# Performance work log

Measured on AMD Instinct MI355X. Metric: run time of the kernel, lower is better.

The kernel has to match this reference:

```python
import jax, jax.numpy as jnp
import numpy as np

N_NODES = 100000
N_EDGES = 1000000
D_IN, H1, H2, D_OUT = 64, 64, 32, 16


def gcn_conv(x, W, b, src, dst, n):
    # PyG GCNConv: add self-loops, symmetric normalization deg^-1/2 A deg^-1/2, then linear.
    h = x @ W  # [N, out]
    ones = jnp.ones(src.shape[0], dtype=x.dtype)
    deg = jax.ops.segment_sum(ones, dst, num_segments=n) + 1.0  # +1 for self-loop
    dinv = jnp.where(deg > 0, jax.lax.rsqrt(deg), 0.0)
    coef = dinv[src] * dinv[dst]  # [E]
    msg = h[src] * coef[:, None]  # [E, out]
    agg = jax.ops.segment_sum(msg, dst, num_segments=n)
    agg = agg + h * (dinv * dinv)[:, None]  # self-loop contribution
    return agg + b


def setup_inputs() -> dict:
    key = jax.random.key(0)
    ks = jax.random.split(key, 16)
    s = 0.1
    inp = {
        "x": jax.random.normal(ks[0], (N_NODES, D_IN), jnp.float32),
        "edge_index": jax.random.randint(ks[1], (2, N_EDGES), 0, N_NODES, jnp.int64),
        # SELayer params
        "U_w": jax.random.normal(ks[2], (D_IN, D_IN), jnp.float32) * s,
        "U_b": jnp.zeros((D_IN,), jnp.float32),
        "fc1_w": jax.random.normal(ks[3], (D_IN, D_IN // 4), jnp.float32) * s,
        "fc1_b": jnp.zeros((D_IN // 4,), jnp.float32),
        "fc2_w": jax.random.normal(ks[4], (D_IN // 4, D_IN), jnp.float32) * s,
        "fc2_b": jnp.zeros((D_IN,), jnp.float32),
        # GCN layers
        "W1": jax.random.normal(ks[5], (D_IN, H1), jnp.float32) * s,
        "b1": jnp.zeros((H1,), jnp.float32),
        "W2": jax.random.normal(ks[6], (H1, H2), jnp.float32) * s,
        "b2": jnp.zeros((H2,), jnp.float32),
        # classifier
        "fc_w": jax.random.normal(ks[7], (H2, D_OUT), jnp.float32) * s,
        "fc_b": jnp.zeros((D_OUT,), jnp.float32),
    }
    return inp


def reference(x, edge_index, U_w, U_b, fc1_w, fc1_b, fc2_w, fc2_b, W1, b1, W2, b2, fc_w, fc_b):
    n = x.shape[0]
    src, dst = edge_index[0], edge_index[1]
    # SE layer
    xu = x @ U_w + U_b
    w = jax.nn.sigmoid(jax.nn.relu(xu @ fc1_w + fc1_b) @ fc2_w + fc2_b)
    h = xu * w
    # GCN stack (dropout is identity in eval mode)
    h = jax.nn.relu(gcn_conv(h, W1, b1, src, dst, n))
    h = jax.nn.relu(gcn_conv(h, W2, b2, src, dst, n))
    logits = h @ fc_w + fc_b
    return jax.nn.log_softmax(logits, axis=1), w
```

## Files before the change

kernel.cpp:

```cpp
#include <hip/hip_runtime.h>
#include <hip/hip_bf16.h>

#define NN 100000
#define NE 1000000
#define CAP 64

#define NPER 196
#define GRID_FAT (NPER * 13)

__device__ __forceinline__ float f4c(const float4& v, int i) {
    switch (i) { case 0: return v.x; case 1: return v.y; case 2: return v.z; default: return v.w; }
}
__device__ __forceinline__ unsigned short f2bf(float f) {
    unsigned u = __float_as_uint(f);
    return (unsigned short)((u + 0x7FFFu + ((u >> 16) & 1u)) >> 16);
}
__device__ __forceinline__ float bf2f(unsigned short s) {
    return __uint_as_float(((unsigned)s) << 16);
}

__global__ __launch_bounds__(256) void zero_k(int* __restrict__ bucket)
{
    long i = (long)blockIdx.x * 256 + threadIdx.x;
    if (i < NN) bucket[i * CAP] = 0;
}

__global__ __launch_bounds__(256) void fat_kernel(
    const float* __restrict__ x, const void* __restrict__ eidx,
    const float* __restrict__ U_w, const float* __restrict__ U_b,
    const float* __restrict__ f1w, const float* __restrict__ f1b,
    const float* __restrict__ f2w, const float* __restrict__ f2b,
    const float* __restrict__ W1,
    int* __restrict__ bucket,
    unsigned short* __restrict__ hW1b, float* __restrict__ w_out)
{
    const int b = blockIdx.x;
    const int r13 = b % 13;
    const int tid = threadIdx.x;

    if (r13 < 5) {
        const int sidx = (b / 13) * 5 + r13;
        long e0 = ((long)sidx * 256 + tid) * 4;
        if (e0 >= NE) return;

        const unsigned* pp = (const unsigned*)eidx;
        bool is64 = true;
#pragma unroll
        for (int k = 0; k < 8; ++k)
            if (pp[2 * k + 1] != 0u) is64 = false;

        int srcs[4], dsts[4];
        if (is64) {
            const long long* p = (const long long*)eidx;
#pragma unroll
            for (int i = 0; i < 4; ++i) {
                srcs[i] = (int)p[e0 + i];
                dsts[i] = (int)p[NE + e0 + i];
            }
        } else {
            const int* p = (const int*)eidx;
            int4 s4 = *(const int4*)&p[e0];
            int4 d4 = *(const int4*)&p[NE + e0];
            srcs[0] = s4.x; srcs[1] = s4.y; srcs[2] = s4.z; srcs[3] = s4.w;
            dsts[0] = d4.x; dsts[1] = d4.y; dsts[2] = d4.z; dsts[3] = d4.w;
        }

        int pos[4];
#pragma unroll
        for (int i = 0; i < 4; ++i) pos[i] = atomicAdd(&bucket[dsts[i] * CAP], 1);
#pragma unroll
        for (int i = 0; i < 4; ++i)
            if (pos[i] < CAP - 1) bucket[dsts[i] * CAP + 1 + pos[i]] = srcs[i];
        return;
    }

    const int seidx = (b / 13) * 8 + (r13 - 5);
    const long base = (long)seidx * 64;
    if (base >= NN) return;

    __shared__ float sU[64][68];
    __shared__ float sx[64][68];
    __shared__ float st1[64][20];
    __shared__ float sUb[64], sb1[16], sb2[64];

    for (int i = tid; i < 1024; i += 256) {
        int r = i >> 4, q = i & 15;
        *(float4*)&sU[r][q * 4] = *(const float4*)&U_w[r * 64 + q * 4];
    }
    for (int i = tid; i < 1024; i += 256) {
        int r = i >> 4, q = i & 15;
        long row = base + r;
        float4 v = make_float4(0.f, 0.f, 0.f, 0.f);
        if (row < NN) v = *(const float4*)&x[row * 64 + q * 4];
        *(float4*)&sx[r][q * 4] = v;
    }
    if (tid < 64) sUb[tid] = U_b[tid];
    if (tid < 16) sb1[tid] = f1b[tid];
    if (tid < 64) sb2[tid] = f2b[tid];
    __syncthreads();

    const int cg = tid & 15, rg = tid >> 4;
    const int r0 = rg * 4, c0 = cg * 4;

    float acc[4][4];
#pragma unroll
    for (int ri = 0; ri < 4; ++ri)
#pragma unroll
        for (int ci = 0; ci < 4; ++ci) acc[ri][ci] = 0.f;

#pragma unroll 4
    for (int kk = 0; kk < 64; kk += 4) {
        float4 xa[4];
#pragma unroll
        for (int ri = 0; ri < 4; ++ri) xa[ri] = *(float4*)&sx[r0 + ri][kk];
#pragma unroll
        for (int kq = 0; kq < 4; ++kq) {
            float4 ub = *(float4*)&sU[kk + kq][c0];
#pragma unroll
            for (int ri = 0; ri < 4; ++ri) {
                float xv = f4c(xa[ri], kq);
                acc[ri][0] = fmaf(xv, ub.x, acc[ri][0]);
                acc[ri][1] = fmaf(xv, ub.y, acc[ri][1]);
                acc[ri][2] = fmaf(xv, ub.z, acc[ri][2]);
                acc[ri][3] = fmaf(xv, ub.w, acc[ri][3]);
            }
        }
    }
    __syncthreads();

#pragma unroll
    for (int ri = 0; ri < 4; ++ri) {
        acc[ri][0] += sUb[c0 + 0];
        acc[ri][1] += sUb[c0 + 1];
        acc[ri][2] += sUb[c0 + 2];
        acc[ri][3] += sUb[c0 + 3];
        float4 o = make_float4(acc[ri][0], acc[ri][1], acc[ri][2], acc[ri][3]);
        *(float4*)&sx[r0 + ri][c0] = o;
    }
    __syncthreads();

    float a1[4] = {sb1[cg], sb1[cg], sb1[cg], sb1[cg]};
#pragma unroll 4
    for (int kk = 0; kk < 64; kk += 4) {
        float4 xa[4];
#pragma unroll
        for (int ri = 0; ri < 4; ++ri) xa[ri] = *(float4*)&sx[r0 + ri][kk];
#pragma unroll
        for (int kq = 0; kq < 4; ++kq) {
            float wv = f1w[(kk + kq) * 16 + cg];
#pragma unroll
            for (int ri = 0; ri < 4; ++ri) a1[ri] = fmaf(f4c(xa[ri], kq), wv, a1[ri]);
        }
    }
#pragma unroll
    for (int ri = 0; ri < 4; ++ri) st1[r0 + ri][cg] = fmaxf(a1[ri], 0.f);
    __syncthreads();

    float a2[4][4];
#pragma unroll
    for (int ri = 0; ri < 4; ++ri)
#pragma unroll
        for (int ci = 0; ci < 4; ++ci) a2[ri][ci] = sb2[c0 + ci];

#pragma unroll
    for (int kk = 0; kk < 16; kk += 4) {
        float4 ta[4];
#pragma unroll
        for (int ri = 0; ri < 4; ++ri) ta[ri] = *(float4*)&st1[r0 + ri][kk];
#pragma unroll
        for (int kq = 0; kq < 4; ++kq) {
            float4 fb = *(const float4*)&f2w[(kk + kq) * 64 + c0];
#pragma unroll
            for (int ri = 0; ri < 4; ++ri) {
                float xv = f4c(ta[ri], kq);
                a2[ri][0] = fmaf(xv, fb.x, a2[ri][0]);
                a2[ri][1] = fmaf(xv, fb.y, a2[ri][1]);
                a2[ri][2] = fmaf(xv, fb.z, a2[ri][2]);
                a2[ri][3] = fmaf(xv, fb.w, a2[ri][3]);
            }
        }
    }
#pragma unroll
    for (int ri = 0; ri < 4; ++ri) {
        long row = base + r0 + ri;
        float4 wv;
        wv.x = 1.f / (1.f + expf(-a2[ri][0]));
        wv.y = 1.f / (1.f + expf(-a2[ri][1]));
        wv.z = 1.f / (1.f + expf(-a2[ri][2]));
        wv.w = 1.f / (1.f + expf(-a2[ri][3]));
        float4 h4;
        h4.x = acc[ri][0] * wv.x; h4.y = acc[ri][1] * wv.y;
        h4.z = acc[ri][2] * wv.z; h4.w = acc[ri][3] * wv.w;
        *(float4*)&sx[r0 + ri][c0] = h4;
        if (row < NN) *(float4*)&w_out[row * 64 + c0] = wv;
    }
    for (int i = tid; i < 1024; i += 256) {
        int r = i >> 4, q = i & 15;
        *(float4*)&sU[r][q * 4] = *(const float4*)&W1[r * 64 + q * 4];
    }
    __syncthreads();

#pragma unroll
    for (int ri = 0; ri < 4; ++ri)
#pragma unroll
        for (int ci = 0; ci < 4; ++ci) acc[ri][ci] = 0.f;

#pragma unroll 4
    for (int kk = 0; kk < 64; kk += 4) {
        float4 xa[4];
#pragma unroll
        for (int ri = 0; ri < 4; ++ri) xa[ri] = *(float4*)&sx[r0 + ri][kk];
#pragma unroll
        for (int kq = 0; kq < 4; ++kq) {
            float4 wb = *(float4*)&sU[kk + kq][c0];
#pragma unroll
            for (int ri = 0; ri < 4; ++ri) {
                float xv = f4c(xa[ri], kq);
                acc[ri][0] = fmaf(xv, wb.x, acc[ri][0]);
                acc[ri][1] = fmaf(xv, wb.y, acc[ri][1]);
                acc[ri][2] = fmaf(xv, wb.z, acc[ri][2]);
                acc[ri][3] = fmaf(xv, wb.w, acc[ri][3]);
            }
        }
    }
#pragma unroll
    for (int ri = 0; ri < 4; ++ri) {
        long row = base + r0 + ri;
        if (row < NN) {
            ushort4 o;
            o.x = f2bf(acc[ri][0]); o.y = f2bf(acc[ri][1]);
            o.z = f2bf(acc[ri][2]); o.w = f2bf(acc[ri][3]);
            *(ushort4*)&hW1b[(size_t)row * 64 + c0] = o;
        }
    }
}

__global__ __launch_bounds__(256) void dinv_k(const int* __restrict__ bucket,
                                              int* __restrict__ cnt,
                                              float* __restrict__ dinv)
{
    long i = (long)blockIdx.x * 256 + threadIdx.x;
    if (i < NN) {
        int c = bucket[i * CAP];
        dinv[i] = rsqrtf((float)c + 1.0f);
        cnt[i] = (c > CAP - 1) ? CAP - 1 : c;
    }
}

__global__ __launch_bounds__(256) void gather64_fused(
    const int* __restrict__ cnt, const int* __restrict__ bucket,
    const float* __restrict__ dinv, const unsigned short* __restrict__ hW1b,
    const float* __restrict__ b1, const float* __restrict__ W2,
    unsigned short* __restrict__ hW2b)
{
    __shared__ float sW2[64 * 32];
    __shared__ float srow[4][64];

    const int tid = threadIdx.x;
    for (int i = tid; i < 512; i += 256)
        *(float4*)&sW2[i * 4] = *(const float4*)&W2[i * 4];

    const int w = tid >> 6;
    const int l = tid & 63;
    const int q = l >> 4;
    const int p = l & 15;
    const long row = (long)blockIdx.x * 4 + w;
    const bool valid = (row < NN);

    int deg = valid ? cnt[row] : 0;
    float dr = valid ? dinv[row] : 0.f;
    const int* bk = bucket + row * CAP + 1;

    int   mysrc = (l < deg) ? bk[l] : 0;
    float mycf  = (l < deg) ? dinv[mysrc] * dr : 0.f;

    float4 acc = make_float4(0.f, 0.f, 0.f, 0.f);
#pragma unroll 2
    for (int e = 0; e < deg; e += 4) {
        int   src = __shfl(mysrc, e + q);
        float cf  = __shfl(mycf,  e + q);
        ushort4 v4 = *(const ushort4*)&hW1b[(size_t)src * 64 + p * 4];
        acc.x = fmaf(bf2f(v4.x), cf, acc.x);
        acc.y = fmaf(bf2f(v4.y), cf, acc.y);
        acc.z = fmaf(bf2f(v4.z), cf, acc.z);
        acc.w = fmaf(bf2f(v4.w), cf, acc.w);
    }
#pragma unroll
    for (int o = 16; o <= 32; o <<= 1) {
        acc.x += __shfl_xor(acc.x, o);
        acc.y += __shfl_xor(acc.y, o);
        acc.z += __shfl_xor(acc.z, o);
        acc.w += __shfl_xor(acc.w, o);
    }
    if (q == 0) {
        ushort4 h4 = valid ? *(const ushort4*)&hW1b[(size_t)row * 64 + p * 4]
                           : make_ushort4(0, 0, 0, 0);
        float4 bb = *(const float4*)&b1[p * 4];
        float dd = dr * dr;
        float4 a1;
        a1.x = fmaxf(fmaf(bf2f(h4.x), dd, bb.x) + acc.x, 0.f);
        a1.y = fmaxf(fmaf(bf2f(h4.y), dd, bb.y) + acc.y, 0.f);
        a1.z = fmaxf(fmaf(bf2f(h4.z), dd, bb.z) + acc.z, 0.f);
        a1.w = fmaxf(fmaf(bf2f(h4.w), dd, bb.w) + acc.w, 0.f);
        *(float4*)&srow[w][p * 4] = a1;
    }
    __syncthreads();

    const int c = l & 31, s = l >> 5;
    float acc2 = 0.f;
#pragma unroll
    for (int kk = 0; kk < 32; ++kk) {
        int k = s * 32 + kk;
        acc2 = fmaf(srow[w][k], sW2[k * 32 + c], acc2);
    }
    acc2 += __shfl_xor(acc2, 32);
    if (s == 0 && valid) hW2b[(size_t)row * 32 + c] = f2bf(acc2);
}

__global__ __launch_bounds__(256) void gather32_fused(
    const int* __restrict__ cnt, const int* __restrict__ bucket,
    const float* __restrict__ dinv, const unsigned short* __restrict__ hW2b,
    const float* __restrict__ b2, const float* __restrict__ fcw,
    const float* __restrict__ fcb, float* __restrict__ out)
{
    __shared__ float sfc[32 * 16];
    __shared__ float srow[4][40];

    const int tid = threadIdx.x;
    for (int i = tid; i < 128; i += 256)
        *(float4*)&sfc[i * 4] = *(const float4*)&fcw[i * 4];

    const int w = tid >> 6;
    const int l = tid & 63;
    const int q = l >> 3;
    const int p = l & 7;
    const long row = (long)blockIdx.x * 4 + w;
    const bool valid = (row < NN);

    int deg = valid ? cnt[row] : 0;
    float dr = valid ? dinv[row] : 0.f;
    const int* bk = bucket + row * CAP + 1;

    int   mysrc = (l < deg) ? bk[l] : 0;
    float mycf  = (l < deg) ? dinv[mysrc] * dr : 0.f;

    float4 acc = make_float4(0.f, 0.f, 0.f, 0.f);
#pragma unroll 2
    for (int e = 0; e < deg; e += 8) {
        int   src = __shfl(mysrc, e + q);
        float cf  = __shfl(mycf,  e + q);
        ushort4 v4 = *(const ushort4*)&hW2b[(size_t)src * 32 + p * 4];
        acc.x = fmaf(bf2f(v4.x), cf, acc.x);
        acc.y = fmaf(bf2f(v4.y), cf, acc.y);
        acc.z = fmaf(bf2f(v4.z), cf, acc.z);
        acc.w = fmaf(bf2f(v4.w), cf, acc.w);
    }
#pragma unroll
    for (int o = 8; o <= 32; o <<= 1) {
        acc.x += __shfl_xor(acc.x, o);
        acc.y += __shfl_xor(acc.y, o);
        acc.z += __shfl_xor(acc.z, o);
        acc.w += __shfl_xor(acc.w, o);
    }
    if (q == 0) {
        ushort4 h4 = valid ? *(const ushort4*)&hW2b[(size_t)row * 32 + p * 4]
                           : make_ushort4(0, 0, 0, 0);
        float4 bb = *(const float4*)&b2[p * 4];
        float dd = dr * dr;
        float4 h2;
        h2.x = fmaxf(fmaf(bf2f(h4.x), dd, bb.x) + acc.x, 0.f);
        h2.y = fmaxf(fmaf(bf2f(h4.y), dd, bb.y) + acc.y, 0.f);
        h2.z = fmaxf(fmaf(bf2f(h4.z), dd, bb.z) + acc.z, 0.f);
        h2.w = fmaxf(fmaf(bf2f(h4.w), dd, bb.w) + acc.w, 0.f);
        *(float4*)&srow[w][p * 4] = h2;
    }
    __syncthreads();

    if (tid < 64) {
        const int r = tid >> 4, c = tid & 15;
        float lg = fcb[c];
#pragma unroll
        for (int k = 0; k < 32; ++k)
            lg = fmaf(srow[r][k], sfc[k * 16 + c], lg);
        float m = lg;
        for (int o = 8; o >= 1; o >>= 1) m = fmaxf(m, __shfl_xor(m, o, 16));
        float ex = expf(lg - m);
        float sum = ex;
        for (int o = 8; o >= 1; o >>= 1) sum += __shfl_xor(sum, o, 16);
        long orow = (long)blockIdx.x * 4 + r;
        if (orow < NN) out[orow * 16 + c] = lg - m - logf(sum);
    }
}

extern "C" void kernel_launch(void* const* d_in, const int* in_sizes, int n_in,
                              void* d_out, int out_size, void* d_ws, size_t ws_size,
                              hipStream_t stream)
{
    const float* x    = (const float*)d_in[0];
    const void*  eidx = d_in[1];
    const float* U_w  = (const float*)d_in[2];
    const float* U_b  = (const float*)d_in[3];
    const float* f1w  = (const float*)d_in[4];
    const float* f1b  = (const float*)d_in[5];
    const float* f2w  = (const float*)d_in[6];
    const float* f2b  = (const float*)d_in[7];
    const float* W1   = (const float*)d_in[8];
    const float* b1   = (const float*)d_in[9];
    const float* W2   = (const float*)d_in[10];
    const float* b2   = (const float*)d_in[11];
    const float* fcw  = (const float*)d_in[12];
    const float* fcb  = (const float*)d_in[13];

    float* out0 = (float*)d_out;
    float* wout = (float*)d_out + 1600000;

    float* ws = (float*)d_ws;

    int*            cnt     = (int*)ws;
    float*          dinv    = ws + 100000;
    int*            bucket  = (int*)(ws + 1800000);
    unsigned short* hW1b    = (unsigned short*)(ws + 8200000);
    unsigned short* hW2b    = (unsigned short*)(ws + 11400000);

    zero_k<<<(NN + 255) / 256, 256, 0, stream>>>(bucket);

    fat_kernel<<<GRID_FAT, 256, 0, stream>>>(x, eidx, U_w, U_b, f1w, f1b, f2w, f2b,
                                             W1, bucket, hW1b, wout);
    dinv_k<<<(NN + 255) / 256, 256, 0, stream>>>(bucket, cnt, dinv);

    gather64_fused<<<NN / 4, 256, 0, stream>>>(cnt, bucket, dinv, hW1b, b1, W2, hW2b);
    gather32_fused<<<NN / 4, 256, 0, stream>>>(cnt, bucket, dinv, hW2b, b2, fcw, fcb, out0);
}
```

Baseline: 182.0 us.

## Interleave edge bucketing with SE compute inside each block

Replaces the split-role fat kernel, where some blocks scattered edges and others ran the SE/GEMM work, with a single block type that does both. Each block loads about 640 edges and issues its atomic slot reservations first, then runs the SE matmul, then writes the bucket entries. The aim is to hide atomic and scatter latency behind the dense compute and to balance work across blocks. In exchange, register pressure rises and edge loads use scalar rather than vectorized accesses.

```diff
diff --git a/kernel.cpp b/kernel.cpp
--- a/kernel.cpp
+++ b/kernel.cpp
@@ -4,9 +4,8 @@
 #define NN 100000
 #define NE 1000000
 #define CAP 64
-
-#define NPER 196
-#define GRID_FAT (NPER * 13)
+#define SE_BLOCKS 1563
+#define EPB 640
 
 __device__ __forceinline__ float f4c(const float4& v, int i) {
     switch (i) { case 0: return v.x; case 1: return v.y; case 2: return v.z; default: return v.w; }
@@ -25,7 +24,7 @@
     if (i < NN) bucket[i * CAP] = 0;
 }
 
-__global__ __launch_bounds__(256) void fat_kernel(
+__global__ __launch_bounds__(256) void se_scat_k(
     const float* __restrict__ x, const void* __restrict__ eidx,
     const float* __restrict__ U_w, const float* __restrict__ U_b,
     const float* __restrict__ f1w, const float* __restrict__ f1b,
@@ -34,49 +33,36 @@
     int* __restrict__ bucket,
     unsigned short* __restrict__ hW1b, float* __restrict__ w_out)
 {
-    const int b = blockIdx.x;
-    const int r13 = b % 13;
     const int tid = threadIdx.x;
-
-    if (r13 < 5) {
-        const int sidx = (b / 13) * 5 + r13;
-        long e0 = ((long)sidx * 256 + tid) * 4;
-        if (e0 >= NE) return;
-
+    const long base = (long)blockIdx.x * 64;
+    const long ebase = (long)blockIdx.x * EPB;
+
+    int esrc[3], edst[3], epos[3];
+    bool ev[3];
+    {
         const unsigned* pp = (const unsigned*)eidx;
         bool is64 = true;
 #pragma unroll
         for (int k = 0; k < 8; ++k)
             if (pp[2 * k + 1] != 0u) is64 = false;
 
-        int srcs[4], dsts[4];
-        if (is64) {
-            const long long* p = (const long long*)eidx;
-#pragma unroll
-            for (int i = 0; i < 4; ++i) {
-                srcs[i] = (int)p[e0 + i];
-                dsts[i] = (int)p[NE + e0 + i];
+        const long long* p64 = (const long long*)eidx;
+        const int* p32 = (const int*)eidx;
+#pragma unroll
+        for (int j = 0; j < 3; ++j) {
+            long idx = (long)j * 256 + tid;
+            long e = ebase + idx;
+            ev[j] = (idx < EPB) && (e < NE);
+            esrc[j] = 0; edst[j] = 0;
+            if (ev[j]) {
+                if (is64) { esrc[j] = (int)p64[e]; edst[j] = (int)p64[NE + e]; }
+                else      { esrc[j] = p32[e];      edst[j] = p32[NE + e]; }
             }
-        } else {
-            const int* p = (const int*)eidx;
-            int4 s4 = *(const int4*)&p[e0];
-            int4 d4 = *(const int4*)&p[NE + e0];
-            srcs[0] = s4.x; srcs[1] = s4.y; srcs[2] = s4.z; srcs[3] = s4.w;
-            dsts[0] = d4.x; dsts[1] = d4.y; dsts[2] = d4.z; dsts[3] = d4.w;
-        }
-
-        int pos[4];
-#pragma unroll
-        for (int i = 0; i < 4; ++i) pos[i] = atomicAdd(&bucket[dsts[i] * CAP], 1);
-#pragma unroll
-        for (int i = 0; i < 4; ++i)
-            if (pos[i] < CAP - 1) bucket[dsts[i] * CAP + 1 + pos[i]] = srcs[i];
-        return;
-    }
-
-    const int seidx = (b / 13) * 8 + (r13 - 5);
-    const long base = (long)seidx * 64;
-    if (base >= NN) return;
+        }
+#pragma unroll
+        for (int j = 0; j < 3; ++j)
+            if (ev[j]) epos[j] = atomicAdd(&bucket[edst[j] * CAP], 1);
+    }
 
     __shared__ float sU[64][68];
     __shared__ float sx[64][68];
@@ -126,6 +112,11 @@
             }
         }
     }
+
+#pragma unroll
+    for (int j = 0; j < 3; ++j)
+        if (ev[j] && epos[j] < CAP - 1) bucket[edst[j] * CAP + 1 + epos[j]] = esrc[j];
+
     __syncthreads();
 
 #pragma unroll
@@ -424,7 +415,7 @@
 
     zero_k<<<(NN + 255) / 256, 256, 0, stream>>>(bucket);
 
-    fat_kernel<<<GRID_FAT, 256, 0, stream>>>(x, eidx, U_w, U_b, f1w, f1b, f2w, f2b,
+    se_scat_k<<<SE_BLOCKS, 256, 0, stream>>>(x, eidx, U_w, U_b, f1w, f1b, f2w, f2b,
                                              W1, bucket, hW1b, wout);
     dinv_k<<<(NN + 255) / 256, 256, 0, stream>>>(bucket, cnt, dinv);
 
```

Result: slower. 199.2 us (+9.5%).
